# Optimization experiments

Hardware: AMD Instinct MI355X
Metric: run time of the kernel (lower is better)

The kernel has to match this reference:

```python
import jax, jax.numpy as jnp
import numpy as np

N_TOTAL = 2_000_000   # total particles across all events
N_EVENTS = 20_000     # number of events (segments)
H = 64                # phi/rho hidden width
OUT = 10              # output classes


def _lin(x, W, b):
    # torch nn.Linear: y = x @ W.T + b
    return x @ W.T + b


def setup_inputs() -> dict:
    key = jax.random.key(0)
    ks = jax.random.split(key, 24)
    s = 0.1  # small init scale
    inp = {
        "values": jax.random.normal(ks[0], (N_TOTAL,), dtype=jnp.float32),
        "seg_ids": jnp.sort(jax.random.randint(ks[1], (N_TOTAL,), 0, N_EVENTS)),
        "p1w0": jax.random.normal(ks[2], (H, 1), dtype=jnp.float32) * s,
        "p1b0": jax.random.normal(ks[3], (H,), dtype=jnp.float32) * s,
        "p1w1": jax.random.normal(ks[4], (H, H), dtype=jnp.float32) * s,
        "p1b1": jax.random.normal(ks[5], (H,), dtype=jnp.float32) * s,
        "r1w0": jax.random.normal(ks[6], (H, H), dtype=jnp.float32) * s,
        "r1b0": jax.random.normal(ks[7], (H,), dtype=jnp.float32) * s,
        "r1w1": jax.random.normal(ks[8], (H, H), dtype=jnp.float32) * s,
        "r1b1": jax.random.normal(ks[9], (H,), dtype=jnp.float32) * s,
        "o1w": jax.random.normal(ks[10], (H, H), dtype=jnp.float32) * s,
        "o1b": jax.random.normal(ks[11], (H,), dtype=jnp.float32) * s,
        "p2w0": jax.random.normal(ks[12], (H, H), dtype=jnp.float32) * s,
        "p2b0": jax.random.normal(ks[13], (H,), dtype=jnp.float32) * s,
        "p2w1": jax.random.normal(ks[14], (H, H), dtype=jnp.float32) * s,
        "p2b1": jax.random.normal(ks[15], (H,), dtype=jnp.float32) * s,
        "r2w0": jax.random.normal(ks[16], (H, H), dtype=jnp.float32) * s,
        "r2b0": jax.random.normal(ks[17], (H,), dtype=jnp.float32) * s,
        "r2w1": jax.random.normal(ks[18], (H, H), dtype=jnp.float32) * s,
        "r2b1": jax.random.normal(ks[19], (H,), dtype=jnp.float32) * s,
        "o2w": jax.random.normal(ks[20], (OUT, H), dtype=jnp.float32) * s,
        "o2b": jax.random.normal(ks[21], (OUT,), dtype=jnp.float32) * s,
    }
    return inp


def reference(values, seg_ids, p1w0, p1b0, p1w1, p1b1, r1w0, r1b0, r1w1, r1b1,
              o1w, o1b, p2w0, p2b0, p2w1, p2b1, r2w0, r2b0, r2w1, r2b1, o2w, o2b):
    relu = jax.nn.relu
    # stage 1: phi1 on each scalar particle value -> [N, H]
    h = relu(_lin(values[:, None], p1w0, p1b0))
    h = relu(_lin(h, p1w1, p1b1))
    # jagged sum over particles within each event (the inner deepset sum)
    ev = jax.ops.segment_sum(h, seg_ids, num_segments=N_EVENTS)  # [E, H]
    # rho1 + output linear + activation per event
    ev = relu(_lin(ev, r1w0, r1b0))
    ev = relu(_lin(ev, r1w1, r1b1))
    ev = relu(_lin(ev, o1w, o1b))  # [E, H] (output_size of deepset1 = rho_sizes[-1])
    # stage 2: phi2 per event, sum over all events
    h2 = relu(_lin(ev, p2w0, p2b0))
    h2 = relu(_lin(h2, p2w1, p2b1))
    s2 = jnp.sum(h2, axis=0, keepdims=True)  # [1, H]
    r2 = relu(_lin(s2, r2w0, r2b0))
    r2 = relu(_lin(r2, r2w1, r2b1))
    out = _lin(r2, o2w, o2b)  # [1, OUT]
    return jax.nn.log_softmax(out, axis=1)
```

## Files before the change

kernel.cpp:

```cpp
#include <hip/hip_runtime.h>

#define NT 2000000
#define NE 20000
#define NTILES (NT / 64)

using bf16x8 = __attribute__((ext_vector_type(8))) __bf16;
using bf16x4 = __attribute__((ext_vector_type(4))) __bf16;
using f32x4  = __attribute__((ext_vector_type(4))) float;
using f32x2  = __attribute__((ext_vector_type(2))) float;
using fvec4  = __attribute__((ext_vector_type(4))) float;

__device__ __forceinline__ void load_bsplit(const float* __restrict__ p,
                                            bf16x8& hi, bf16x8& lo) {
    fvec4 a = *(const fvec4*)p;
    fvec4 b = *(const fvec4*)(p + 4);
#pragma unroll
    for (int e = 0; e < 4; e++) {
        float v  = a[e];
        __bf16 h = (__bf16)v;
        hi[e]    = h;
        lo[e]    = (__bf16)(v - (float)h);
        float v2  = b[e];
        __bf16 h2 = (__bf16)v2;
        hi[e + 4] = h2;
        lo[e + 4] = (__bf16)(v2 - (float)h2);
    }
}

__device__ __forceinline__ bf16x8 load_bf8(const float* __restrict__ p) {
    fvec4 a = *(const fvec4*)p;
    fvec4 b = *(const fvec4*)(p + 4);
    bf16x8 r;
#pragma unroll
    for (int e = 0; e < 4; e++) {
        r[e]     = (__bf16)a[e];
        r[e + 4] = (__bf16)b[e];
    }
    return r;
}

__global__ __launch_bounds__(256, 4) void k1_phi1(
    const float* __restrict__ values, const int* __restrict__ seg,
    const float* __restrict__ w0, const float* __restrict__ b0,
    const float* __restrict__ w1, const float* __restrict__ b1,
    float* __restrict__ ev) {
    const int tid = threadIdx.x;
    const int w   = tid >> 6;
    const int l   = tid & 63;
    const int l15 = l & 15;
    const int l4  = l >> 4;

    bf16x8 Bh[2][4];
#pragma unroll
    for (int kf = 0; kf < 2; kf++)
#pragma unroll
        for (int jf = 0; jf < 4; jf++)
            Bh[kf][jf] = load_bf8(w1 + (jf * 16 + l15) * 64 + kf * 32 + l4 * 8);

    f32x2 w0p[2][4], b0p[2][4];
#pragma unroll
    for (int kf = 0; kf < 2; kf++) {
        const int kb = kf * 32 + l4 * 8;
#pragma unroll
        for (int e2 = 0; e2 < 4; e2++) {
            w0p[kf][e2] = *(const f32x2*)(w0 + kb + e2 * 2);
            b0p[kf][e2] = *(const f32x2*)(b0 + kb + e2 * 2);
        }
    }
    f32x4 biasC[4];
#pragma unroll
    for (int jf = 0; jf < 4; jf++) {
        const float bj = b1[jf * 16 + l15];
#pragma unroll
        for (int r = 0; r < 4; r++) biasC[jf][r] = bj;
    }

    const bool bit0 = (l & 16) != 0;
    const bool bit1 = (l & 32) != 0;
    auto reduce4 = [&](const float sj[4]) -> float {
        float send01 = bit0 ? sj[0] : sj[1];
        float keep01 = bit0 ? sj[1] : sj[0];
        float c01 = keep01 + __shfl_xor(send01, 16);
        float send23 = bit0 ? sj[2] : sj[3];
        float keep23 = bit0 ? sj[3] : sj[2];
        float c23 = keep23 + __shfl_xor(send23, 16);
        float send = bit1 ? c01 : c23;
        float keep = bit1 ? c23 : c01;
        return keep + __shfl_xor(send, 32);
    };

    const int stride = gridDim.x * 4;
    int tile = blockIdx.x * 4 + w;

    int s_cur = seg[tile * 64 + l];
    float vp[4];
#pragma unroll
    for (int pf = 0; pf < 4; pf++) vp[pf] = values[tile * 64 + pf * 16 + l15];

    while (tile < NTILES) {
        const int ntile = tile + stride;
        int s_nxt = 0;
        float vpn[4] = {0.f, 0.f, 0.f, 0.f};
        if (ntile < NTILES) {
            const int nb = ntile * 64;
            s_nxt = seg[nb + l];
#pragma unroll
            for (int pf = 0; pf < 4; pf++) vpn[pf] = values[nb + pf * 16 + l15];
        }

        const int prev = __shfl_up(s_cur, 1);
        const unsigned long long bmask = __ballot((l > 0) && (s_cur != prev));

        int   cur = __builtin_amdgcn_readlane(s_cur, 0);
        float sj[4] = {0.f, 0.f, 0.f, 0.f};

#pragma unroll
        for (int q = 0; q < 2; q++) {
#pragma unroll
            for (int i = 0; i < 2; i++) {
                const int B = q * 32 + i * 16;
                const float vq = vp[2 * q + i];
                const f32x2 vv = {vq, vq};

                bf16x8 A0, A1;
#pragma unroll
                for (int e2 = 0; e2 < 4; e2++) {
                    f32x2 h0 = w0p[0][e2] * vv + b0p[0][e2];
                    A0[2 * e2]     = (__bf16)fmaxf(h0[0], 0.f);
                    A0[2 * e2 + 1] = (__bf16)fmaxf(h0[1], 0.f);
                    f32x2 h1 = w0p[1][e2] * vv + b0p[1][e2];
                    A1[2 * e2]     = (__bf16)fmaxf(h1[0], 0.f);
                    A1[2 * e2 + 1] = (__bf16)fmaxf(h1[1], 0.f);
                }

                f32x4 frag[4];
#pragma unroll
                for (int jf = 0; jf < 4; jf++) {
                    f32x4 t = __builtin_amdgcn_mfma_f32_16x16x32_bf16(
                        A0, Bh[0][jf], biasC[jf], 0, 0, 0);
                    t = __builtin_amdgcn_mfma_f32_16x16x32_bf16(
                        A1, Bh[1][jf], t, 0, 0, 0);
#pragma unroll
                    for (int r = 0; r < 4; r++) frag[jf][r] = fmaxf(t[r], 0.f);
                }

                const unsigned int mb =
                    (unsigned int)((bmask >> B) & 0xFFFFull);
                if (mb == 0u) {
#pragma unroll
                    for (int jf = 0; jf < 4; jf++)
                        sj[jf] += (frag[jf][0] + frag[jf][1]) +
                                  (frag[jf][2] + frag[jf][3]);
                } else {
                    unsigned int m = mb;
                    int start = 0;
                    while (true) {
                        const int e = m ? (int)__builtin_ctz(m) : 16;
#pragma unroll
                        for (int jf = 0; jf < 4; jf++) {
                            float s = 0.f;
#pragma unroll
                            for (int r = 0; r < 4; r++) {
                                const int rel = l4 * 4 + r;
                                s += (rel >= start && rel < e) ? frag[jf][r]
                                                               : 0.f;
                            }
                            sj[jf] += s;
                        }
                        if (!m) break;
                        atomicAdd(ev + (size_t)cur * 64 + l, reduce4(sj));
                        sj[0] = sj[1] = sj[2] = sj[3] = 0.f;
                        cur   = __builtin_amdgcn_readlane(s_cur, B + e);
                        start = e;
                        m &= (m - 1);
                    }
                }
            }
        }
        atomicAdd(ev + (size_t)cur * 64 + l, reduce4(sj));

        tile  = ntile;
        s_cur = s_nxt;
#pragma unroll
        for (int pf = 0; pf < 4; pf++) vp[pf] = vpn[pf];
    }
}

__global__ __launch_bounds__(64) void k2_events(
    const float* __restrict__ ev,
    const float* __restrict__ W0, const float* __restrict__ B0,
    const float* __restrict__ W1, const float* __restrict__ B1,
    const float* __restrict__ W2, const float* __restrict__ B2,
    const float* __restrict__ W3, const float* __restrict__ B3,
    const float* __restrict__ W4, const float* __restrict__ B4,
    float* __restrict__ s2) {
    __shared__ __align__(16) __bf16 xt[64 * 72];
    const int l   = threadIdx.x;
    const int l15 = l & 15;
    const int l4  = l >> 4;
    const int ebase = blockIdx.x * 64;

    const float* Ws[5] = {W0, W1, W2, W3, W4};
    const float* Bs[5] = {B0, B1, B2, B3, B4};

    bf16x8 A[4][2];
#pragma unroll
    for (int pf = 0; pf < 4; pf++) {
        const int e = ebase + pf * 16 + l15;
#pragma unroll
        for (int kf = 0; kf < 2; kf++) {
            bf16x8 a;
            if (e < NE) {
                const float* p = ev + (size_t)e * 64 + kf * 32 + l4 * 8;
                fvec4 x = *(const fvec4*)p;
                fvec4 y = *(const fvec4*)(p + 4);
#pragma unroll
                for (int e2 = 0; e2 < 4; e2++) {
                    a[e2]     = (__bf16)x[e2];
                    a[e2 + 4] = (__bf16)y[e2];
                }
            } else {
#pragma unroll
                for (int e2 = 0; e2 < 8; e2++) a[e2] = (__bf16)0.f;
            }
            A[pf][kf] = a;
        }
    }

#pragma unroll
    for (int L = 0; L < 5; L++) {
        bf16x8 Bh[2][4], Bl[2][4];
#pragma unroll
        for (int kf = 0; kf < 2; kf++)
#pragma unroll
            for (int jf = 0; jf < 4; jf++)
                load_bsplit(Ws[L] + (jf * 16 + l15) * 64 + kf * 32 + l4 * 8,
                            Bh[kf][jf], Bl[kf][jf]);

        f32x4 acc[4][4];
#pragma unroll
        for (int jf = 0; jf < 4; jf++) {
            const float bj = Bs[L][jf * 16 + l15];
#pragma unroll
            for (int pf = 0; pf < 4; pf++)
#pragma unroll
                for (int r = 0; r < 4; r++) acc[pf][jf][r] = bj;
        }
#pragma unroll
        for (int kf = 0; kf < 2; kf++)
#pragma unroll
            for (int pf = 0; pf < 4; pf++)
#pragma unroll
                for (int jf = 0; jf < 4; jf++)
                    acc[pf][jf] = __builtin_amdgcn_mfma_f32_16x16x32_bf16(
                        A[pf][kf], Bh[kf][jf], acc[pf][jf], 0, 0, 0);
#pragma unroll
        for (int kf = 0; kf < 2; kf++)
#pragma unroll
            for (int pf = 0; pf < 4; pf++)
#pragma unroll
                for (int jf = 0; jf < 4; jf++)
                    acc[pf][jf] = __builtin_amdgcn_mfma_f32_16x16x32_bf16(
                        A[pf][kf], Bl[kf][jf], acc[pf][jf], 0, 0, 0);

        if (L < 4) {
#pragma unroll
            for (int pf = 0; pf < 4; pf++)
#pragma unroll
                for (int jf = 0; jf < 4; jf++) {
                    const int j = jf * 16 + l15;
#pragma unroll
                    for (int r = 0; r < 4; r++)
                        xt[(pf * 16 + l4 * 4 + r) * 72 + j] =
                            (__bf16)fmaxf(acc[pf][jf][r], 0.f);
                }
#pragma unroll
            for (int pf = 0; pf < 4; pf++)
#pragma unroll
                for (int kf = 0; kf < 2; kf++)
                    A[pf][kf] = *(const bf16x8*)(xt + (pf * 16 + l15) * 72 +
                                                 kf * 32 + l4 * 8);
        } else {
            float sj[4];
#pragma unroll
            for (int jf = 0; jf < 4; jf++) {
                float s = 0.f;
#pragma unroll
                for (int pf = 0; pf < 4; pf++)
#pragma unroll
                    for (int r = 0; r < 4; r++) {
                        const int e = ebase + pf * 16 + l4 * 4 + r;
                        float v = fmaxf(acc[pf][jf][r], 0.f);
                        s += (e < NE) ? v : 0.f;
                    }
                s += __shfl_xor(s, 16);
                s += __shfl_xor(s, 32);
                sj[jf] = s;
            }
            float v = (l4 == 0) ? sj[0] : (l4 == 1) ? sj[1]
                    : (l4 == 2) ? sj[2] : sj[3];
            atomicAdd(s2 + l, v);
        }
    }
}

__global__ __launch_bounds__(64) void k3_final(
    const float* __restrict__ s2,
    const float* __restrict__ W0, const float* __restrict__ B0,
    const float* __restrict__ W1, const float* __restrict__ B1,
    const float* __restrict__ W2, const float* __restrict__ B2,
    float* __restrict__ out) {
    __shared__ __align__(16) float xb[64];
    __shared__ __align__(16) float yb[64];
    __shared__ float ob[10];
    const int l = threadIdx.x;

    xb[l] = s2[l];
    __syncthreads();

    float a = B0[l];
#pragma unroll
    for (int k = 0; k < 16; k++) {
        fvec4 wv = *(const fvec4*)(W0 + l * 64 + k * 4);
        fvec4 xv = *(const fvec4*)(xb + k * 4);
        a += wv[0] * xv[0] + wv[1] * xv[1] + wv[2] * xv[2] + wv[3] * xv[3];
    }
    yb[l] = fmaxf(a, 0.f);
    __syncthreads();

    float b_ = B1[l];
#pragma unroll
    for (int k = 0; k < 16; k++) {
        fvec4 wv = *(const fvec4*)(W1 + l * 64 + k * 4);
        fvec4 xv = *(const fvec4*)(yb + k * 4);
        b_ += wv[0] * xv[0] + wv[1] * xv[1] + wv[2] * xv[2] + wv[3] * xv[3];
    }
    __syncthreads();
    xb[l] = fmaxf(b_, 0.f);
    __syncthreads();

    if (l < 10) {
        float o = B2[l];
#pragma unroll
        for (int k = 0; k < 16; k++) {
            fvec4 wv = *(const fvec4*)(W2 + l * 64 + k * 4);
            fvec4 xv = *(const fvec4*)(xb + k * 4);
            o += wv[0] * xv[0] + wv[1] * xv[1] + wv[2] * xv[2] + wv[3] * xv[3];
        }
        ob[l] = o;
    }
    __syncthreads();
    if (l == 0) {
        float m = ob[0];
#pragma unroll
        for (int i = 1; i < 10; i++) m = fmaxf(m, ob[i]);
        float sum = 0.f;
#pragma unroll
        for (int i = 0; i < 10; i++) sum = sum + expf(ob[i] - m);
        float ls = logf(sum);
#pragma unroll
        for (int i = 0; i < 10; i++) out[i] = ob[i] - m - ls;
    }
}

extern "C" void kernel_launch(void* const* d_in, const int* in_sizes, int n_in,
                              void* d_out, int out_size, void* d_ws, size_t ws_size,
                              hipStream_t stream) {
    const float* values = (const float*)d_in[0];
    const int*   seg    = (const int*)d_in[1];
    const float* p1w0 = (const float*)d_in[2],  *p1b0 = (const float*)d_in[3];
    const float* p1w1 = (const float*)d_in[4],  *p1b1 = (const float*)d_in[5];
    const float* r1w0 = (const float*)d_in[6],  *r1b0 = (const float*)d_in[7];
    const float* r1w1 = (const float*)d_in[8],  *r1b1 = (const float*)d_in[9];
    const float* o1w  = (const float*)d_in[10], *o1b  = (const float*)d_in[11];
    const float* p2w0 = (const float*)d_in[12], *p2b0 = (const float*)d_in[13];
    const float* p2w1 = (const float*)d_in[14], *p2b1 = (const float*)d_in[15];
    const float* r2w0 = (const float*)d_in[16], *r2b0 = (const float*)d_in[17];
    const float* r2w1 = (const float*)d_in[18], *r2b1 = (const float*)d_in[19];
    const float* o2w  = (const float*)d_in[20], *o2b  = (const float*)d_in[21];

    float* ev = (float*)d_ws;
    float* s2 = ev + (size_t)NE * 64;

    hipMemsetAsync(d_ws, 0, (size_t)(NE * 64 + 64) * sizeof(float), stream);

    hipLaunchKernelGGL(k1_phi1, dim3(1024), dim3(256), 0, stream,
                       values, seg, p1w0, p1b0, p1w1, p1b1, ev);
    hipLaunchKernelGGL(k2_events, dim3((NE + 63) / 64), dim3(64), 0, stream,
                       ev, r1w0, r1b0, r1w1, r1b1, o1w, o1b,
                       p2w0, p2b0, p2w1, p2b1, s2);
    hipLaunchKernelGGL(k3_final, dim3(1), dim3(64), 0, stream,
                       s2, r2w0, r2b0, r2w1, r2b1, o2w, o2b, (float*)d_out);
}
```

Measured before the change: 73.65 us.

## Use contiguous per-wave tile ranges, fp16 MFMA, and staged segment flushes

Each wave now processes a contiguous range of tiles, so a segment's partial sum carries across tile boundaries instead of being flushed with an atomic at the end of every tile. Segment partials are written to a staging buffer, and a separate combine kernel applies the atomics to the event array. It falls back to direct atomics if the workspace is too small. The phi1 math also moves from bf16 to fp16 MFMA, with the first layer computed in packed half precision. This adds an extra kernel launch and staging traffic, and fp16 has less dynamic range than bf16, so accuracy could suffer.

After: 73.00 us. No clear change (-0.9%).

```diff
diff --git a/kernel.cpp b/kernel.cpp
--- a/kernel.cpp
+++ b/kernel.cpp
@@ -3,9 +3,15 @@
 #define NT 2000000
 #define NE 20000
 #define NTILES (NT / 64)
+#define K1_BLOCKS 1024
+#define K1_WAVES (K1_BLOCKS * 4)
+#define TILES_BASE (NTILES / K1_WAVES)
+#define TILES_REM (NTILES - TILES_BASE * K1_WAVES)
+#define STAGE_CAP 24
 
 using bf16x8 = __attribute__((ext_vector_type(8))) __bf16;
-using bf16x4 = __attribute__((ext_vector_type(4))) __bf16;
+using half8  = __attribute__((ext_vector_type(8))) _Float16;
+using half2v = __attribute__((ext_vector_type(2))) _Float16;
 using f32x4  = __attribute__((ext_vector_type(4))) float;
 using f32x2  = __attribute__((ext_vector_type(2))) float;
 using fvec4  = __attribute__((ext_vector_type(4))) float;
@@ -27,14 +33,14 @@
     }
 }
 
-__device__ __forceinline__ bf16x8 load_bf8(const float* __restrict__ p) {
+__device__ __forceinline__ half8 load_h8(const float* __restrict__ p) {
     fvec4 a = *(const fvec4*)p;
     fvec4 b = *(const fvec4*)(p + 4);
-    bf16x8 r;
+    half8 r;
 #pragma unroll
     for (int e = 0; e < 4; e++) {
-        r[e]     = (__bf16)a[e];
-        r[e + 4] = (__bf16)b[e];
+        r[e]     = (_Float16)a[e];
+        r[e + 4] = (_Float16)b[e];
     }
     return r;
 }
@@ -43,28 +49,32 @@
     const float* __restrict__ values, const int* __restrict__ seg,
     const float* __restrict__ w0, const float* __restrict__ b0,
     const float* __restrict__ w1, const float* __restrict__ b1,
-    float* __restrict__ ev) {
+    float* __restrict__ ev,
+    float* __restrict__ stage, int* __restrict__ sid_arr,
+    int* __restrict__ cnt_arr, int use_stage) {
     const int tid = threadIdx.x;
     const int w   = tid >> 6;
     const int l   = tid & 63;
     const int l15 = l & 15;
     const int l4  = l >> 4;
 
-    bf16x8 Bh[2][4];
+    half8 Bh[2][4];
 #pragma unroll
     for (int kf = 0; kf < 2; kf++)
 #pragma unroll
         for (int jf = 0; jf < 4; jf++)
-            Bh[kf][jf] = load_bf8(w1 + (jf * 16 + l15) * 64 + kf * 32 + l4 * 8);
-
-    f32x2 w0p[2][4], b0p[2][4];
+            Bh[kf][jf] = load_h8(w1 + (jf * 16 + l15) * 64 + kf * 32 + l4 * 8);
+
+    half2v w0h[2][4], b0h[2][4];
 #pragma unroll
     for (int kf = 0; kf < 2; kf++) {
         const int kb = kf * 32 + l4 * 8;
 #pragma unroll
         for (int e2 = 0; e2 < 4; e2++) {
-            w0p[kf][e2] = *(const f32x2*)(w0 + kb + e2 * 2);
-            b0p[kf][e2] = *(const f32x2*)(b0 + kb + e2 * 2);
+            f32x2 wp = *(const f32x2*)(w0 + kb + 2 * e2);
+            f32x2 bp = *(const f32x2*)(b0 + kb + 2 * e2);
+            w0h[kf][e2] = half2v{(_Float16)wp[0], (_Float16)wp[1]};
+            b0h[kf][e2] = half2v{(_Float16)bp[0], (_Float16)bp[1]};
         }
     }
     f32x4 biasC[4];
@@ -89,100 +99,128 @@
         return keep + __shfl_xor(send, 32);
     };
 
-    const int stride = gridDim.x * 4;
-    int tile = blockIdx.x * 4 + w;
-
-    int s_cur = seg[tile * 64 + l];
-    float vp[4];
-#pragma unroll
-    for (int pf = 0; pf < 4; pf++) vp[pf] = values[tile * 64 + pf * 16 + l15];
-
-    while (tile < NTILES) {
-        const int ntile = tile + stride;
+    const int wid   = blockIdx.x * 4 + w;
+    const int start = wid * TILES_BASE + (wid < TILES_REM ? wid : TILES_REM);
+    const int end   = start + TILES_BASE + (wid < TILES_REM ? 1 : 0);
+
+    int nf = 0;
+    auto FLUSH = [&](int sid, float* sj) {
+        const float v = reduce4(sj);
+        if (use_stage && nf < STAGE_CAP) {
+            const int slot = wid * STAGE_CAP + nf;
+            stage[(size_t)slot * 64 + l] = v;
+            if (l == 0) sid_arr[slot] = sid;
+            nf++;
+        } else {
+            atomicAdd(ev + (size_t)sid * 64 + l, v);
+        }
+    };
+
+    int t = start;
+    int s_cur = seg[t * 64 + l];
+    half2v vph[2];
+#pragma unroll
+    for (int b = 0; b < 4; b++)
+        vph[b >> 1][b & 1] = (_Float16)values[t * 64 + b * 16 + l15];
+
+    int   cur = __builtin_amdgcn_readlane(s_cur, 0);
+    float sj[4] = {0.f, 0.f, 0.f, 0.f};
+
+    while (t < end) {
+        const int nt = t + 1;
         int s_nxt = 0;
-        float vpn[4] = {0.f, 0.f, 0.f, 0.f};
-        if (ntile < NTILES) {
-            const int nb = ntile * 64;
-            s_nxt = seg[nb + l];
-#pragma unroll
-            for (int pf = 0; pf < 4; pf++) vpn[pf] = values[nb + pf * 16 + l15];
+        half2v vpn[2];
+#pragma unroll
+        for (int i = 0; i < 2; i++) vpn[i] = half2v{(_Float16)0.f, (_Float16)0.f};
+        if (nt < end) {
+            s_nxt = seg[nt * 64 + l];
+#pragma unroll
+            for (int b = 0; b < 4; b++)
+                vpn[b >> 1][b & 1] = (_Float16)values[nt * 64 + b * 16 + l15];
         }
 
         const int prev = __shfl_up(s_cur, 1);
-        const unsigned long long bmask = __ballot((l > 0) && (s_cur != prev));
-
-        int   cur = __builtin_amdgcn_readlane(s_cur, 0);
-        float sj[4] = {0.f, 0.f, 0.f, 0.f};
-
-#pragma unroll
-        for (int q = 0; q < 2; q++) {
-#pragma unroll
-            for (int i = 0; i < 2; i++) {
-                const int B = q * 32 + i * 16;
-                const float vq = vp[2 * q + i];
-                const f32x2 vv = {vq, vq};
-
-                bf16x8 A0, A1;
-#pragma unroll
-                for (int e2 = 0; e2 < 4; e2++) {
-                    f32x2 h0 = w0p[0][e2] * vv + b0p[0][e2];
-                    A0[2 * e2]     = (__bf16)fmaxf(h0[0], 0.f);
-                    A0[2 * e2 + 1] = (__bf16)fmaxf(h0[1], 0.f);
-                    f32x2 h1 = w0p[1][e2] * vv + b0p[1][e2];
-                    A1[2 * e2]     = (__bf16)fmaxf(h1[0], 0.f);
-                    A1[2 * e2 + 1] = (__bf16)fmaxf(h1[1], 0.f);
-                }
-
-                f32x4 frag[4];
-#pragma unroll
-                for (int jf = 0; jf < 4; jf++) {
-                    f32x4 t = __builtin_amdgcn_mfma_f32_16x16x32_bf16(
-                        A0, Bh[0][jf], biasC[jf], 0, 0, 0);
-                    t = __builtin_amdgcn_mfma_f32_16x16x32_bf16(
-                        A1, Bh[1][jf], t, 0, 0, 0);
-#pragma unroll
-                    for (int r = 0; r < 4; r++) frag[jf][r] = fmaxf(t[r], 0.f);
-                }
-
-                const unsigned int mb =
-                    (unsigned int)((bmask >> B) & 0xFFFFull);
-                if (mb == 0u) {
-#pragma unroll
-                    for (int jf = 0; jf < 4; jf++)
-                        sj[jf] += (frag[jf][0] + frag[jf][1]) +
-                                  (frag[jf][2] + frag[jf][3]);
-                } else {
-                    unsigned int m = mb;
-                    int start = 0;
-                    while (true) {
-                        const int e = m ? (int)__builtin_ctz(m) : 16;
-#pragma unroll
-                        for (int jf = 0; jf < 4; jf++) {
-                            float s = 0.f;
-#pragma unroll
-                            for (int r = 0; r < 4; r++) {
-                                const int rel = l4 * 4 + r;
-                                s += (rel >= start && rel < e) ? frag[jf][r]
-                                                               : 0.f;
-                            }
-                            sj[jf] += s;
+        const bool diff = (l == 0) ? (s_cur != cur) : (s_cur != prev);
+        const unsigned long long mask = __ballot(diff);
+
+#pragma unroll
+        for (int b = 0; b < 4; b++) {
+            const unsigned mask16 = (unsigned)((mask >> (16 * b)) & 0xFFFFull);
+            const _Float16 vh = vph[b >> 1][b & 1];
+            const half2v vv = {vh, vh};
+
+            half8 A0, A1;
+#pragma unroll
+            for (int e2 = 0; e2 < 4; e2++) {
+                half2v h0 = vv * w0h[0][e2] + b0h[0][e2];
+                half2v h1 = vv * w0h[1][e2] + b0h[1][e2];
+                const _Float16 z = (_Float16)0.f;
+                A0[2 * e2]     = h0[0] > z ? h0[0] : z;
+                A0[2 * e2 + 1] = h0[1] > z ? h0[1] : z;
+                A1[2 * e2]     = h1[0] > z ? h1[0] : z;
+                A1[2 * e2 + 1] = h1[1] > z ? h1[1] : z;
+            }
+
+            f32x4 frag[4];
+#pragma unroll
+            for (int jf = 0; jf < 4; jf++) {
+                f32x4 tt = __builtin_amdgcn_mfma_f32_16x16x32_f16(
+                    A0, Bh[0][jf], biasC[jf], 0, 0, 0);
+                tt = __builtin_amdgcn_mfma_f32_16x16x32_f16(
+                    A1, Bh[1][jf], tt, 0, 0, 0);
+#pragma unroll
+                for (int r = 0; r < 4; r++) frag[jf][r] = fmaxf(tt[r], 0.f);
+            }
+
+            if (mask16 == 0u) {
+#pragma unroll
+                for (int jf = 0; jf < 4; jf++)
+                    sj[jf] += (frag[jf][0] + frag[jf][1]) +
+                              (frag[jf][2] + frag[jf][3]);
+            } else {
+                unsigned m = mask16;
+                int st = 0;
+                while (true) {
+                    const int e = m ? (int)__builtin_ctz(m) : 16;
+#pragma unroll
+                    for (int jf = 0; jf < 4; jf++) {
+                        float s = 0.f;
+#pragma unroll
+                        for (int r = 0; r < 4; r++) {
+                            const int rel = l4 * 4 + r;
+                            s += (rel >= st && rel < e) ? frag[jf][r] : 0.f;
                         }
-                        if (!m) break;
-                        atomicAdd(ev + (size_t)cur * 64 + l, reduce4(sj));
-                        sj[0] = sj[1] = sj[2] = sj[3] = 0.f;
-                        cur   = __builtin_amdgcn_readlane(s_cur, B + e);
-                        start = e;
-                        m &= (m - 1);
+                        sj[jf] += s;
                     }
+                    if (!m) break;
+                    FLUSH(cur, sj);
+                    sj[0] = sj[1] = sj[2] = sj[3] = 0.f;
+                    cur = __builtin_amdgcn_readlane(s_cur, 16 * b + e);
+                    st  = e;
+                    m &= (m - 1);
                 }
             }
         }
-        atomicAdd(ev + (size_t)cur * 64 + l, reduce4(sj));
-
-        tile  = ntile;
+
+        t = nt;
         s_cur = s_nxt;
-#pragma unroll
-        for (int pf = 0; pf < 4; pf++) vp[pf] = vpn[pf];
+        vph[0] = vpn[0];
+        vph[1] = vpn[1];
+    }
+    FLUSH(cur, sj);
+    if (use_stage && l == 0) cnt_arr[wid] = nf;
+}
+
+__global__ __launch_bounds__(256) void k1_combine(
+    const float* __restrict__ stage, const int* __restrict__ sid_arr,
+    const int* __restrict__ cnt_arr, float* __restrict__ ev) {
+    const int w = threadIdx.x >> 6, l = threadIdx.x & 63;
+    const int wid = blockIdx.x * 4 + w;
+    const int n = cnt_arr[wid];
+    for (int c = 0; c < n; ++c) {
+        const int slot = wid * STAGE_CAP + c;
+        const int sid  = sid_arr[slot];
+        atomicAdd(ev + (size_t)sid * 64 + l, stage[(size_t)slot * 64 + l]);
     }
 }
 
@@ -381,11 +419,25 @@
 
     float* ev = (float*)d_ws;
     float* s2 = ev + (size_t)NE * 64;
+    int*   cnt_arr = (int*)(s2 + 64);
+    int*   sid_arr = cnt_arr + K1_WAVES;
+    float* stage   = (float*)(sid_arr + (size_t)K1_WAVES * STAGE_CAP);
+
+    const size_t need = ((size_t)NE * 64 + 64) * 4 +
+                        (size_t)K1_WAVES * 4 +
+                        (size_t)K1_WAVES * STAGE_CAP * 4 +
+                        (size_t)K1_WAVES * STAGE_CAP * 64 * 4;
+    const int use_stage = (ws_size >= need) ? 1 : 0;
 
     hipMemsetAsync(d_ws, 0, (size_t)(NE * 64 + 64) * sizeof(float), stream);
 
-    hipLaunchKernelGGL(k1_phi1, dim3(1024), dim3(256), 0, stream,
-                       values, seg, p1w0, p1b0, p1w1, p1b1, ev);
+    hipLaunchKernelGGL(k1_phi1, dim3(K1_BLOCKS), dim3(256), 0, stream,
+                       values, seg, p1w0, p1b0, p1w1, p1b1, ev,
+                       stage, sid_arr, cnt_arr, use_stage);
+    if (use_stage) {
+        hipLaunchKernelGGL(k1_combine, dim3(K1_WAVES / 4), dim3(256), 0, stream,
+                           stage, sid_arr, cnt_arr, ev);
+    }
     hipLaunchKernelGGL(k2_events, dim3((NE + 63) / 64), dim3(64), 0, stream,
                        ev, r1w0, r1b0, r1w1, r1b1, o1w, o1b,
                        p2w0, p2b0, p2w1, p2b1, s2);
```
